# Performance work log

Hardware: AMD Instinct MI355X
Metric: run time of the kernel (lower is better)

Reference implementation:

```python
import jax, jax.numpy as jnp
import numpy as np

IN, E, BSZ, A, J, NC, BATCH = 784, 512, 8, 2, 7, 128, 512
T = BSZ ** A  # 64 blocks


def setup_inputs() -> dict:
    key = jax.random.key(0)
    ks = jax.random.split(key, 10)
    s = lambda k, sh: (jax.random.normal(k, sh, jnp.float32) * 0.02)
    return {
        "x": jax.random.normal(ks[0], (BATCH, IN), jnp.float32),
        "emb_W": s(ks[1], (IN, E)), "emb_b": jnp.zeros((E,), jnp.float32),
        # stacked per-block state_transform: Linear(E,E)-ReLU-Linear(E,E)-ReLU
        "st_W1": s(ks[2], (T, E, E)), "st_b1": jnp.zeros((T, E), jnp.float32),
        "st_W2": s(ks[3], (T, E, E)), "st_b2": jnp.zeros((T, E), jnp.float32),
        # stacked per-block address_transform: Linear(E,E)-ReLU-Linear(E,A*BSZ)
        "ad_W1": s(ks[4], (T, E, E)), "ad_b1": jnp.zeros((T, E), jnp.float32),
        "ad_W2": s(ks[5], (T, E, A * BSZ)), "ad_b2": jnp.zeros((T, A * BSZ), jnp.float32),
        # output head: Linear(E,E)-ReLU-Linear(E,NC)
        "out_W1": s(ks[6], (E, E)), "out_b1": jnp.zeros((E,), jnp.float32),
        "out_W2": s(ks[7], (E, NC)), "out_b2": jnp.zeros((NC,), jnp.float32),
    }


def reference(x, emb_W, emb_b, st_W1, st_b1, st_W2, st_b2,
              ad_W1, ad_b1, ad_W2, ad_b2, out_W1, out_b1, out_W2, out_b2):
    strides = BSZ ** jnp.arange(A - 1, -1, -1)  # row-major flat index

    def flat_idx(addr):  # [B, A] -> [B]
        return jnp.sum(addr * strides, axis=1)

    def next_address(state, idx):
        # block's address_transform; argmax(softmax(logits)) == argmax(logits)
        h = jax.nn.relu(jnp.einsum("be,beh->bh", state, ad_W1[idx]) + ad_b1[idx])
        logits = jnp.einsum("bh,bho->bo", h, ad_W2[idx]) + ad_b2[idx]
        return jnp.argmax(logits.reshape(-1, A, BSZ), axis=2)  # [B, A]

    def through_block(state, idx):
        h = jax.nn.relu(jnp.einsum("be,beh->bh", state, st_W1[idx]) + st_b1[idx])
        t = jax.nn.relu(jnp.einsum("bh,bho->bo", h, st_W2[idx]) + st_b2[idx])
        norm = jnp.linalg.norm(state, axis=1, keepdims=True)
        return t / (norm + 1e-6)

    state = x.reshape(x.shape[0], -1) @ emb_W + emb_b  # [B, E]
    initial_state = state
    B = state.shape[0]
    # initial address from brain_blocks[0]
    addr = next_address(initial_state, jnp.zeros((B,), jnp.int32))

    for i in range(J):  # small fixed jump count
        idx = flat_idx(addr)
        t = through_block(state, idx)           # normalized transformed state
        addr = next_address(t, idx)             # address from transformed state
        state = t + (i / max(1, J - 1)) * initial_state  # residual ramp

    final = through_block(state, flat_idx(addr)) + initial_state
    h = jax.nn.relu(final @ out_W1 + out_b1)
    return h @ out_W2 + out_b2  # [B, NC]
```

## Files before the change

kernel.cpp:

```cpp
#include <hip/hip_runtime.h>

namespace {

constexpr int B     = 512;
constexpr int IN_F  = 784;
constexpr int E     = 512;
constexpr int ABSZ  = 16;
constexpr int J     = 7;
constexpr int NC    = 128;
constexpr int NT    = 256;

__device__ inline void matvec512(const float* __restrict__ W,
                                 const float* __restrict__ bias,
                                 const float* __restrict__ vin,
                                 float* __restrict__ vout,
                                 int tid, bool do_relu)
{
    const int o = 2 * tid;
    float a0 = 0.f, a1 = 0.f;
    const float* wp = W + o;
    #pragma unroll 8
    for (int e = 0; e < E; ++e) {
        const float v = vin[e];
        const float2 w = *reinterpret_cast<const float2*>(wp + (size_t)e * E);
        a0 = fmaf(v, w.x, a0);
        a1 = fmaf(v, w.y, a1);
    }
    a0 += bias[o];
    a1 += bias[o + 1];
    if (do_relu) { a0 = fmaxf(a0, 0.f); a1 = fmaxf(a1, 0.f); }
    vout[o]     = a0;
    vout[o + 1] = a1;
}

__device__ inline int next_address(const float* __restrict__ ad_W1,
                                   const float* __restrict__ ad_b1,
                                   const float* __restrict__ ad_W2,
                                   const float* __restrict__ ad_b2,
                                   int idx,
                                   const float* __restrict__ vin,
                                   float* __restrict__ s_h,
                                   float* __restrict__ s_part,
                                   float* __restrict__ s_logits,
                                   int* __restrict__ s_idx_p,
                                   int tid)
{
    matvec512(ad_W1 + (size_t)idx * E * E, ad_b1 + (size_t)idx * E, vin, s_h, tid, true);
    __syncthreads();

    {
        const int o  = tid & (ABSZ - 1);
        const int e0 = tid >> 4;
        const float* w2 = ad_W2 + (size_t)idx * E * ABSZ;
        float acc = 0.f;
        #pragma unroll 4
        for (int e = e0; e < E; e += 16) {
            acc = fmaf(s_h[e], w2[(size_t)e * ABSZ + o], acc);
        }
        s_part[tid] = acc;
    }
    __syncthreads();
    if (tid < ABSZ) {
        float sum = ad_b2[(size_t)idx * ABSZ + tid];
        #pragma unroll
        for (int k = 0; k < 16; ++k) sum += s_part[tid + 16 * k];
        s_logits[tid] = sum;
    }
    __syncthreads();
    if (tid == 0) {
        int a0 = 0, a1 = 0;
        float m0 = s_logits[0], m1 = s_logits[8];
        #pragma unroll
        for (int k = 1; k < 8; ++k) {
            if (s_logits[k]     > m0) { m0 = s_logits[k];     a0 = k; }
            if (s_logits[8 + k] > m1) { m1 = s_logits[8 + k]; a1 = k; }
        }
        *s_idx_p = a0 * 8 + a1;
    }
    __syncthreads();
    return *s_idx_p;
}

__device__ inline void through_block(const float* __restrict__ st_W1,
                                     const float* __restrict__ st_b1,
                                     const float* __restrict__ st_W2,
                                     const float* __restrict__ st_b2,
                                     int idx,
                                     const float* __restrict__ s_state,
                                     float* __restrict__ s_h,
                                     float* __restrict__ s_t,
                                     float* __restrict__ s_part,
                                     float* __restrict__ s_scale,
                                     int tid)
{
    matvec512(st_W1 + (size_t)idx * E * E, st_b1 + (size_t)idx * E, s_state, s_h, tid, true);

    {
        const int o = 2 * tid;
        float v0 = s_state[o], v1 = s_state[o + 1];
        float ss = v0 * v0 + v1 * v1;
        #pragma unroll
        for (int off = 32; off > 0; off >>= 1) ss += __shfl_down(ss, off, 64);
        if ((tid & 63) == 0) s_part[tid >> 6] = ss;
    }
    __syncthreads();
    if (tid == 0) {
        float tot = s_part[0] + s_part[1] + s_part[2] + s_part[3];
        *s_scale = 1.0f / (sqrtf(tot) + 1e-6f);
    }
    matvec512(st_W2 + (size_t)idx * E * E, st_b2 + (size_t)idx * E, s_h, s_t, tid, true);
    __syncthreads();
    {
        const float sc = *s_scale;
        const int o = 2 * tid;
        s_t[o]     *= sc;
        s_t[o + 1] *= sc;
    }
    __syncthreads();
}

__global__ __launch_bounds__(NT) void brain_kernel(
    const float* __restrict__ x,
    const float* __restrict__ emb_W,  const float* __restrict__ emb_b,
    const float* __restrict__ st_W1,  const float* __restrict__ st_b1,
    const float* __restrict__ st_W2,  const float* __restrict__ st_b2,
    const float* __restrict__ ad_W1,  const float* __restrict__ ad_b1,
    const float* __restrict__ ad_W2,  const float* __restrict__ ad_b2,
    const float* __restrict__ out_W1, const float* __restrict__ out_b1,
    const float* __restrict__ out_W2, const float* __restrict__ out_b2,
    float* __restrict__ out)
{
    const int b   = blockIdx.x;
    const int tid = threadIdx.x;

    __shared__ float s_x[IN_F];
    __shared__ float s_state[E];
    __shared__ float s_init[E];
    __shared__ float s_h[E];
    __shared__ float s_t[E];
    __shared__ float s_part[NT];
    __shared__ float s_logits[ABSZ];
    __shared__ float s_scale;
    __shared__ int   s_idx;

    for (int i = tid; i < IN_F; i += NT) s_x[i] = x[(size_t)b * IN_F + i];
    __syncthreads();

    {
        const int o = 2 * tid;
        float a0 = 0.f, a1 = 0.f;
        const float* wp = emb_W + o;
        #pragma unroll 4
        for (int i = 0; i < IN_F; ++i) {
            const float v = s_x[i];
            const float2 w = *reinterpret_cast<const float2*>(wp + (size_t)i * E);
            a0 = fmaf(v, w.x, a0);
            a1 = fmaf(v, w.y, a1);
        }
        a0 += emb_b[o];
        a1 += emb_b[o + 1];
        s_state[o]     = a0;  s_state[o + 1] = a1;
        s_init[o]      = a0;  s_init[o + 1]  = a1;
    }
    __syncthreads();

    int idx = next_address(ad_W1, ad_b1, ad_W2, ad_b2, 0, s_init,
                           s_h, s_part, s_logits, &s_idx, tid);

    for (int i = 0; i < J; ++i) {
        through_block(st_W1, st_b1, st_W2, st_b2, idx,
                      s_state, s_h, s_t, s_part, &s_scale, tid);
        const int nidx = next_address(ad_W1, ad_b1, ad_W2, ad_b2, idx, s_t,
                                      s_h, s_part, s_logits, &s_idx, tid);
        {
            const float ramp = (float)i * (1.0f / 6.0f);
            const int o = 2 * tid;
            s_state[o]     = s_t[o]     + ramp * s_init[o];
            s_state[o + 1] = s_t[o + 1] + ramp * s_init[o + 1];
        }
        __syncthreads();
        idx = nidx;
    }

    through_block(st_W1, st_b1, st_W2, st_b2, idx,
                  s_state, s_h, s_t, s_part, &s_scale, tid);
    {
        const int o = 2 * tid;
        s_state[o]     = s_t[o]     + s_init[o];
        s_state[o + 1] = s_t[o + 1] + s_init[o + 1];
    }
    __syncthreads();

    matvec512(out_W1, out_b1, s_state, s_h, tid, true);
    __syncthreads();

    {
        const int oo = tid & (NC - 1);
        const int e0 = tid >> 7;
        float acc = 0.f;
        #pragma unroll 4
        for (int e = e0; e < E; e += 2) {
            acc = fmaf(s_h[e], out_W2[(size_t)e * NC + oo], acc);
        }
        s_part[tid] = acc;
    }
    __syncthreads();
    if (tid < NC) {
        out[(size_t)b * NC + tid] = out_b2[tid] + s_part[tid] + s_part[tid + NC];
    }
}

}

extern "C" void kernel_launch(void* const* d_in, const int* in_sizes, int n_in,
                              void* d_out, int out_size, void* d_ws, size_t ws_size,
                              hipStream_t stream)
{
    const float* x      = (const float*)d_in[0];
    const float* emb_W  = (const float*)d_in[1];
    const float* emb_b  = (const float*)d_in[2];
    const float* st_W1  = (const float*)d_in[3];
    const float* st_b1  = (const float*)d_in[4];
    const float* st_W2  = (const float*)d_in[5];
    const float* st_b2  = (const float*)d_in[6];
    const float* ad_W1  = (const float*)d_in[7];
    const float* ad_b1  = (const float*)d_in[8];
    const float* ad_W2  = (const float*)d_in[9];
    const float* ad_b2  = (const float*)d_in[10];
    const float* out_W1 = (const float*)d_in[11];
    const float* out_b1 = (const float*)d_in[12];
    const float* out_W2 = (const float*)d_in[13];
    const float* out_b2 = (const float*)d_in[14];
    float* out = (float*)d_out;

    hipLaunchKernelGGL(brain_kernel, dim3(B), dim3(NT), 0, stream,
                       x, emb_W, emb_b, st_W1, st_b1, st_W2, st_b2,
                       ad_W1, ad_b1, ad_W2, ad_b2,
                       out_W1, out_b1, out_W2, out_b2, out);
}
```

Measured before the change: 1.755 ms.

## Bucket rows by block index and run persistent cooperative kernel with 8-row tiled matvecs

Replaces the one-workgroup-per-sample kernel with a persistent cooperative kernel that runs stage by stage, separated by grid syncs. Before each jump it buckets samples by their chosen block index, so each workgroup processes up to 8 rows that share the same weight matrix and reuses every loaded weight column across those rows. This cuts the redundant weight streaming the per-sample approach incurred. In exchange it adds many grid-wide barriers, global workspace traffic for intermediate activations, and partially filled tiles when buckets are small.

```diff
diff --git a/kernel.cpp b/kernel.cpp
--- a/kernel.cpp
+++ b/kernel.cpp
@@ -1,212 +1,361 @@
 #include <hip/hip_runtime.h>
+#include <hip/hip_cooperative_groups.h>
+
+namespace cg = cooperative_groups;
 
 namespace {
 
-constexpr int B     = 512;
-constexpr int IN_F  = 784;
-constexpr int E     = 512;
-constexpr int ABSZ  = 16;
-constexpr int J     = 7;
-constexpr int NC    = 128;
-constexpr int NT    = 256;
-
-__device__ inline void matvec512(const float* __restrict__ W,
-                                 const float* __restrict__ bias,
-                                 const float* __restrict__ vin,
-                                 float* __restrict__ vout,
-                                 int tid, bool do_relu)
-{
-    const int o = 2 * tid;
-    float a0 = 0.f, a1 = 0.f;
-    const float* wp = W + o;
-    #pragma unroll 8
-    for (int e = 0; e < E; ++e) {
-        const float v = vin[e];
-        const float2 w = *reinterpret_cast<const float2*>(wp + (size_t)e * E);
-        a0 = fmaf(v, w.x, a0);
-        a1 = fmaf(v, w.y, a1);
-    }
-    a0 += bias[o];
-    a1 += bias[o + 1];
-    if (do_relu) { a0 = fmaxf(a0, 0.f); a1 = fmaxf(a1, 0.f); }
-    vout[o]     = a0;
-    vout[o + 1] = a1;
-}
-
-__device__ inline int next_address(const float* __restrict__ ad_W1,
-                                   const float* __restrict__ ad_b1,
-                                   const float* __restrict__ ad_W2,
-                                   const float* __restrict__ ad_b2,
-                                   int idx,
-                                   const float* __restrict__ vin,
-                                   float* __restrict__ s_h,
-                                   float* __restrict__ s_part,
-                                   float* __restrict__ s_logits,
-                                   int* __restrict__ s_idx_p,
-                                   int tid)
-{
-    matvec512(ad_W1 + (size_t)idx * E * E, ad_b1 + (size_t)idx * E, vin, s_h, tid, true);
+constexpr int Bn   = 512;
+constexpr int INF  = 784;
+constexpr int E    = 512;
+constexpr int Tn   = 64;
+constexpr int ABSZ = 16;
+constexpr int Jn   = 7;
+constexpr int NC   = 128;
+constexpr int NT   = 256;
+constexpr int DESCMAX = 128;
+
+struct Params {
+    const float *x, *emb_W, *emb_b;
+    const float *st_W1, *st_b1, *st_W2, *st_b2;
+    const float *ad_W1, *ad_b1, *ad_W2, *ad_b2;
+    const float *out_W1, *out_b1, *out_W2, *out_b2;
+    float *out;
+    float *state, *initv, *hbuf, *tbuf, *norms;
+    int *idx, *g_rlist;
+    int4 *g_desc;
+};
+
+__device__ inline void stage_rows(const float* __restrict__ in, int instride,
+                                  int kb, int klen, const int* rid,
+                                  float (*s_in)[E], int tid)
+{
+    #pragma unroll
+    for (int g = 0; g < 8; ++g) {
+        const float* src = in + (size_t)rid[g] * instride + kb;
+        float* dst = s_in[g];
+        for (int e4 = tid; e4 < (klen >> 2); e4 += NT)
+            reinterpret_cast<float4*>(dst)[e4] =
+                reinterpret_cast<const float4*>(src)[e4];
+    }
+}
+
+__device__ inline void accum8(const float* __restrict__ Wp,
+                              const float (*s_in)[E], int klen, float acc[8])
+{
+    #pragma unroll 2
+    for (int e = 0; e < klen; e += 4) {
+        const float w0 = Wp[(size_t)(e + 0) * E];
+        const float w1 = Wp[(size_t)(e + 1) * E];
+        const float w2 = Wp[(size_t)(e + 2) * E];
+        const float w3 = Wp[(size_t)(e + 3) * E];
+        #pragma unroll
+        for (int g = 0; g < 8; ++g) {
+            const float4 f = *reinterpret_cast<const float4*>(&s_in[g][e]);
+            acc[g] = fmaf(f.x, w0, acc[g]);
+            acc[g] = fmaf(f.y, w1, acc[g]);
+            acc[g] = fmaf(f.z, w2, acc[g]);
+            acc[g] = fmaf(f.w, w3, acc[g]);
+        }
+    }
+}
+
+__device__ inline int build_buckets(const int* __restrict__ gidx,
+                                    int* cnt, int* off, int* rk, int* tb,
+                                    int* rlist, int4* sdesc,
+                                    int tid, bool pub, const Params& P)
+{
+    if (tid < Tn) { cnt[tid] = 0; rk[tid] = 0; }
     __syncthreads();
-
-    {
-        const int o  = tid & (ABSZ - 1);
-        const int e0 = tid >> 4;
-        const float* w2 = ad_W2 + (size_t)idx * E * ABSZ;
-        float acc = 0.f;
-        #pragma unroll 4
-        for (int e = e0; e < E; e += 16) {
-            acc = fmaf(s_h[e], w2[(size_t)e * ABSZ + o], acc);
-        }
-        s_part[tid] = acc;
-    }
-    __syncthreads();
-    if (tid < ABSZ) {
-        float sum = ad_b2[(size_t)idx * ABSZ + tid];
-        #pragma unroll
-        for (int k = 0; k < 16; ++k) sum += s_part[tid + 16 * k];
-        s_logits[tid] = sum;
-    }
+    int rv[2];
+    #pragma unroll
+    for (int k = 0; k < 2; ++k) rv[k] = gidx[tid + k * NT];
+    #pragma unroll
+    for (int k = 0; k < 2; ++k) atomicAdd(&cnt[rv[k]], 1);
     __syncthreads();
     if (tid == 0) {
-        int a0 = 0, a1 = 0;
-        float m0 = s_logits[0], m1 = s_logits[8];
-        #pragma unroll
-        for (int k = 1; k < 8; ++k) {
-            if (s_logits[k]     > m0) { m0 = s_logits[k];     a0 = k; }
-            if (s_logits[8 + k] > m1) { m1 = s_logits[8 + k]; a1 = k; }
-        }
-        *s_idx_p = a0 * 8 + a1;
+        int s = 0, t = 0;
+        for (int b = 0; b < Tn; ++b) {
+            off[b] = s; tb[b] = t;
+            s += cnt[b]; t += (cnt[b] + 7) >> 3;
+        }
+        tb[Tn] = t;
     }
     __syncthreads();
-    return *s_idx_p;
-}
-
-__device__ inline void through_block(const float* __restrict__ st_W1,
-                                     const float* __restrict__ st_b1,
-                                     const float* __restrict__ st_W2,
-                                     const float* __restrict__ st_b2,
-                                     int idx,
-                                     const float* __restrict__ s_state,
-                                     float* __restrict__ s_h,
-                                     float* __restrict__ s_t,
-                                     float* __restrict__ s_part,
-                                     float* __restrict__ s_scale,
-                                     int tid)
-{
-    matvec512(st_W1 + (size_t)idx * E * E, st_b1 + (size_t)idx * E, s_state, s_h, tid, true);
+    #pragma unroll
+    for (int k = 0; k < 2; ++k) {
+        const int r = tid + k * NT, b = rv[k];
+        rlist[off[b] + atomicAdd(&rk[b], 1)] = r;
+    }
+    __syncthreads();
+    const int nt = tb[Tn];
+    for (int t = tid; t < DESCMAX; t += NT) {
+        int4 d = make_int4(0, 0, 0, 0);
+        if (t < nt) {
+            int b = 0;
+            while (tb[b + 1] <= t) ++b;
+            const int j = t - tb[b];
+            d = make_int4(b, off[b] + j * 8, min(8, cnt[b] - j * 8), 0);
+        }
+        sdesc[t] = d;
+    }
+    __syncthreads();
+    if (pub) {
+        for (int r = tid; r < Bn; r += NT) P.g_rlist[r] = rlist[r];
+        for (int t = tid; t < DESCMAX; t += NT) P.g_desc[t] = sdesc[t];
+    }
+    return nt;
+}
+
+enum { EPI_EMBED, EPI_H, EPI_T, EPI_FINAL };
+
+template <int EPI>
+__device__ void stage_mv(const Params& P, const float* __restrict__ in,
+                         int instride, int K,
+                         const float* __restrict__ W, const float* __restrict__ bias,
+                         bool gathered, int ntiles,
+                         const int* __restrict__ rl, const int4* __restrict__ dsc,
+                         float* __restrict__ outp,
+                         float (*s_in)[E], int tid, int bid, int gridn)
+{
+    const int items = ntiles * 2;
+    for (int s = bid; s < items; s += gridn) {
+        const int tile = s >> 1, chunk = s & 1;
+        int blk = 0, start = tile * 8, n = 8;
+        if (gathered) {
+            const int4 d = dsc[tile];
+            blk = d.x; start = d.y; n = d.z;
+            if (n == 0) continue;
+        }
+        int rid[8];
+        #pragma unroll
+        for (int g = 0; g < 8; ++g)
+            rid[g] = gathered ? rl[start + min(g, n - 1)] : (start + g);
+
+        float acc[8] = {0, 0, 0, 0, 0, 0, 0, 0};
+        for (int kb = 0; kb < K; kb += E) {
+            const int klen = min(E, K - kb);
+            __syncthreads();
+            stage_rows(in, instride, kb, klen, rid, s_in, tid);
+            __syncthreads();
+            const float* Wp = W + (size_t)blk * K * E + (size_t)kb * E
+                              + (chunk * NT + tid);
+            accum8(Wp, s_in, klen, acc);
+        }
+        const int c = chunk * NT + tid;
+        const float bv = bias[(gathered ? blk * E : 0) + c];
+        #pragma unroll
+        for (int g = 0; g < 8; ++g) {
+            if (g < n) {
+                float v = acc[g] + bv;
+                const size_t o = (size_t)rid[g] * E + c;
+                if (EPI == EPI_EMBED) {
+                    P.state[o] = v; P.initv[o] = v;
+                } else if (EPI == EPI_H) {
+                    outp[o] = fmaxf(v, 0.f);
+                } else if (EPI == EPI_T) {
+                    outp[o] = fmaxf(v, 0.f) / (P.norms[rid[g]] + 1e-6f);
+                } else {
+                    P.state[o] = fmaxf(v, 0.f) / (P.norms[rid[g]] + 1e-6f)
+                                 + P.initv[o];
+                }
+            }
+        }
+    }
+}
+
+template <bool UPDATE>
+__device__ void stage_addr(const Params& P, const float* __restrict__ in,
+                           float ramp, bool gathered, int ntiles,
+                           const int* __restrict__ rl, const int4* __restrict__ dsc,
+                           float (*s_in)[E], float* slog,
+                           int tid, int bid, int gridn)
+{
+    for (int s = bid; s < ntiles; s += gridn) {
+        int blk = 0, start = s * 8, n = 8;
+        if (gathered) {
+            const int4 d = dsc[s];
+            blk = d.x; start = d.y; n = d.z;
+            if (n == 0) continue;
+        }
+        int rid[8];
+        #pragma unroll
+        for (int g = 0; g < 8; ++g)
+            rid[g] = gathered ? rl[start + min(g, n - 1)] : (start + g);
+
+        __syncthreads();
+        stage_rows(in, E, 0, E, rid, s_in, tid);
+        __syncthreads();
+
+        const float* W1 = P.ad_W1 + (size_t)blk * E * E;
+        float a0[8] = {0, 0, 0, 0, 0, 0, 0, 0};
+        float a1[8] = {0, 0, 0, 0, 0, 0, 0, 0};
+        #pragma unroll 2
+        for (int e = 0; e < E; e += 4) {
+            float w0[4], w1v[4];
+            #pragma unroll
+            for (int q = 0; q < 4; ++q) {
+                w0[q]  = W1[(size_t)(e + q) * E + tid];
+                w1v[q] = W1[(size_t)(e + q) * E + tid + NT];
+            }
+            #pragma unroll
+            for (int g = 0; g < 8; ++g) {
+                const float4 f = *reinterpret_cast<const float4*>(&s_in[g][e]);
+                a0[g] = fmaf(f.x, w0[0], a0[g]);
+                a0[g] = fmaf(f.y, w0[1], a0[g]);
+                a0[g] = fmaf(f.z, w0[2], a0[g]);
+                a0[g] = fmaf(f.w, w0[3], a0[g]);
+                a1[g] = fmaf(f.x, w1v[0], a1[g]);
+                a1[g] = fmaf(f.y, w1v[1], a1[g]);
+                a1[g] = fmaf(f.z, w1v[2], a1[g]);
+                a1[g] = fmaf(f.w, w1v[3], a1[g]);
+            }
+        }
+
+        {
+            const int g = tid >> 5, l = tid & 31;
+            if (g < n) {
+                const int r = rid[g];
+                float ss = 0.f;
+                const int e0 = l * 16;
+                #pragma unroll
+                for (int e = e0; e < e0 + 16; e += 4) {
+                    float4 tv = *reinterpret_cast<const float4*>(&s_in[g][e]);
+                    if (UPDATE) {
+                        const float4 iv = *reinterpret_cast<const float4*>(
+                            &P.initv[(size_t)r * E + e]);
+                        tv.x = fmaf(ramp, iv.x, tv.x);
+                        tv.y = fmaf(ramp, iv.y, tv.y);
+                        tv.z = fmaf(ramp, iv.z, tv.z);
+                        tv.w = fmaf(ramp, iv.w, tv.w);
+                        *reinterpret_cast<float4*>(&P.state[(size_t)r * E + e]) = tv;
+                    }
+                    ss += tv.x * tv.x + tv.y * tv.y + tv.z * tv.z + tv.w * tv.w;
+                }
+                #pragma unroll
+                for (int m = 16; m > 0; m >>= 1) ss += __shfl_xor(ss, m, 64);
+                if (l == 0) P.norms[r] = sqrtf(ss);
+            }
+        }
+        __syncthreads();
+
+        const float bb0 = P.ad_b1[blk * E + tid];
+        const float bb1 = P.ad_b1[blk * E + tid + NT];
+        #pragma unroll
+        for (int g = 0; g < 8; ++g) {
+            s_in[g][tid]      = fmaxf(a0[g] + bb0, 0.f);
+            s_in[g][tid + NT] = fmaxf(a1[g] + bb1, 0.f);
+        }
+        __syncthreads();
+
+        {
+            const int d = tid >> 1, half = tid & 1;
+            const int row = d >> 4, o = d & 15;
+            const float* W2 = P.ad_W2 + (size_t)blk * E * ABSZ;
+            float lacc = 0.f;
+            const int e0 = half * 256;
+            #pragma unroll 4
+            for (int e = e0; e < e0 + 256; ++e)
+                lacc = fmaf(s_in[row][e], W2[(size_t)e * ABSZ + o], lacc);
+            lacc += __shfl_xor(lacc, 1, 64);
+            if (half == 0) slog[d] = lacc + P.ad_b2[blk * ABSZ + o];
+        }
+        __syncthreads();
+        if (tid < n) {
+            const float* L = slog + tid * ABSZ;
+            int A0 = 0, A1 = 0;
+            float m0 = L[0], m1 = L[8];
+            #pragma unroll
+            for (int k = 1; k < 8; ++k) {
+                if (L[k]     > m0) { m0 = L[k];     A0 = k; }
+                if (L[8 + k] > m1) { m1 = L[8 + k]; A1 = k; }
+            }
+            P.idx[rid[tid]] = A0 * 8 + A1;
+        }
+        __syncthreads();
+    }
+}
+
+__global__ __launch_bounds__(NT, 2) void brain_fused(Params P)
+{
+    cg::grid_group grid = cg::this_grid();
+    const int tid = threadIdx.x, bid = blockIdx.x, gridn = gridDim.x;
+
+    __shared__ float s_in[8][E];
+    __shared__ int   rlist[Bn];
+    __shared__ int4  sdesc[DESCMAX];
+    __shared__ int   cnt[Tn], off[Tn], rk[Tn], tb[Tn + 1];
+    __shared__ float slog[8 * ABSZ];
+
+    stage_mv<EPI_EMBED>(P, P.x, INF, INF, P.emb_W, P.emb_b,
+                        false, Bn / 8, nullptr, nullptr, nullptr,
+                        s_in, tid, bid, gridn);
+    grid.sync();
+
+    stage_addr<false>(P, P.initv, 0.f, false, Bn / 8, nullptr, nullptr,
+                      s_in, slog, tid, bid, gridn);
+    grid.sync();
+
+    for (int i = 0; i < Jn; ++i) {
+        const int nt = build_buckets(P.idx, cnt, off, rk, tb, rlist, sdesc,
+                                     tid, bid == 0, P);
+        stage_mv<EPI_H>(P, P.state, E, E, P.st_W1, P.st_b1,
+                        true, nt, rlist, sdesc, P.hbuf,
+                        s_in, tid, bid, gridn);
+        grid.sync();
+        stage_mv<EPI_T>(P, P.hbuf, E, E, P.st_W2, P.st_b2,
+                        true, nt, P.g_rlist, P.g_desc, P.tbuf,
+                        s_in, tid, bid, gridn);
+        grid.sync();
+        stage_addr<true>(P, P.tbuf, (float)i * (1.0f / 6.0f),
+                         true, nt, P.g_rlist, P.g_desc,
+                         s_in, slog, tid, bid, gridn);
+        grid.sync();
+    }
 
     {
-        const int o = 2 * tid;
-        float v0 = s_state[o], v1 = s_state[o + 1];
-        float ss = v0 * v0 + v1 * v1;
-        #pragma unroll
-        for (int off = 32; off > 0; off >>= 1) ss += __shfl_down(ss, off, 64);
-        if ((tid & 63) == 0) s_part[tid >> 6] = ss;
-    }
-    __syncthreads();
-    if (tid == 0) {
-        float tot = s_part[0] + s_part[1] + s_part[2] + s_part[3];
-        *s_scale = 1.0f / (sqrtf(tot) + 1e-6f);
-    }
-    matvec512(st_W2 + (size_t)idx * E * E, st_b2 + (size_t)idx * E, s_h, s_t, tid, true);
-    __syncthreads();
-    {
-        const float sc = *s_scale;
-        const int o = 2 * tid;
-        s_t[o]     *= sc;
-        s_t[o + 1] *= sc;
-    }
-    __syncthreads();
-}
-
-__global__ __launch_bounds__(NT) void brain_kernel(
-    const float* __restrict__ x,
-    const float* __restrict__ emb_W,  const float* __restrict__ emb_b,
-    const float* __restrict__ st_W1,  const float* __restrict__ st_b1,
-    const float* __restrict__ st_W2,  const float* __restrict__ st_b2,
-    const float* __restrict__ ad_W1,  const float* __restrict__ ad_b1,
-    const float* __restrict__ ad_W2,  const float* __restrict__ ad_b2,
-    const float* __restrict__ out_W1, const float* __restrict__ out_b1,
-    const float* __restrict__ out_W2, const float* __restrict__ out_b2,
-    float* __restrict__ out)
-{
-    const int b   = blockIdx.x;
-    const int tid = threadIdx.x;
-
-    __shared__ float s_x[IN_F];
-    __shared__ float s_state[E];
-    __shared__ float s_init[E];
-    __shared__ float s_h[E];
-    __shared__ float s_t[E];
-    __shared__ float s_part[NT];
-    __shared__ float s_logits[ABSZ];
-    __shared__ float s_scale;
-    __shared__ int   s_idx;
-
-    for (int i = tid; i < IN_F; i += NT) s_x[i] = x[(size_t)b * IN_F + i];
-    __syncthreads();
-
-    {
-        const int o = 2 * tid;
-        float a0 = 0.f, a1 = 0.f;
-        const float* wp = emb_W + o;
+        const int nt = build_buckets(P.idx, cnt, off, rk, tb, rlist, sdesc,
+                                     tid, bid == 0, P);
+        stage_mv<EPI_H>(P, P.state, E, E, P.st_W1, P.st_b1,
+                        true, nt, rlist, sdesc, P.hbuf,
+                        s_in, tid, bid, gridn);
+        grid.sync();
+        stage_mv<EPI_FINAL>(P, P.hbuf, E, E, P.st_W2, P.st_b2,
+                            true, nt, P.g_rlist, P.g_desc, nullptr,
+                            s_in, tid, bid, gridn);
+        grid.sync();
+    }
+
+    stage_mv<EPI_H>(P, P.state, E, E, P.out_W1, P.out_b1,
+                    false, Bn / 8, nullptr, nullptr, P.hbuf,
+                    s_in, tid, bid, gridn);
+    grid.sync();
+
+    for (int s = bid; s < Bn / 8; s += gridn) {
+        const int base = s * 8;
+        int rid[8];
+        #pragma unroll
+        for (int g = 0; g < 8; ++g) rid[g] = base + g;
+        __syncthreads();
+        stage_rows(P.hbuf, E, 0, E, rid, s_in, tid);
+        __syncthreads();
+        const int col = tid & (NC - 1), rg = tid >> 7;
+        float acc[4] = {0, 0, 0, 0};
         #pragma unroll 4
-        for (int i = 0; i < IN_F; ++i) {
-            const float v = s_x[i];
-            const float2 w = *reinterpret_cast<const float2*>(wp + (size_t)i * E);
-            a0 = fmaf(v, w.x, a0);
-            a1 = fmaf(v, w.y, a1);
-        }
-        a0 += emb_b[o];
-        a1 += emb_b[o + 1];
-        s_state[o]     = a0;  s_state[o + 1] = a1;
-        s_init[o]      = a0;  s_init[o + 1]  = a1;
-    }
-    __syncthreads();
-
-    int idx = next_address(ad_W1, ad_b1, ad_W2, ad_b2, 0, s_init,
-                           s_h, s_part, s_logits, &s_idx, tid);
-
-    for (int i = 0; i < J; ++i) {
-        through_block(st_W1, st_b1, st_W2, st_b2, idx,
-                      s_state, s_h, s_t, s_part, &s_scale, tid);
-        const int nidx = next_address(ad_W1, ad_b1, ad_W2, ad_b2, idx, s_t,
-                                      s_h, s_part, s_logits, &s_idx, tid);
-        {
-            const float ramp = (float)i * (1.0f / 6.0f);
-            const int o = 2 * tid;
-            s_state[o]     = s_t[o]     + ramp * s_init[o];
-            s_state[o + 1] = s_t[o + 1] + ramp * s_init[o + 1];
-        }
-        __syncthreads();
-        idx = nidx;
-    }
-
-    through_block(st_W1, st_b1, st_W2, st_b2, idx,
-                  s_state, s_h, s_t, s_part, &s_scale, tid);
-    {
-        const int o = 2 * tid;
-        s_state[o]     = s_t[o]     + s_init[o];
-        s_state[o + 1] = s_t[o + 1] + s_init[o + 1];
-    }
-    __syncthreads();
-
-    matvec512(out_W1, out_b1, s_state, s_h, tid, true);
-    __syncthreads();
-
-    {
-        const int oo = tid & (NC - 1);
-        const int e0 = tid >> 7;
-        float acc = 0.f;
-        #pragma unroll 4
-        for (int e = e0; e < E; e += 2) {
-            acc = fmaf(s_h[e], out_W2[(size_t)e * NC + oo], acc);
-        }
-        s_part[tid] = acc;
-    }
-    __syncthreads();
-    if (tid < NC) {
-        out[(size_t)b * NC + tid] = out_b2[tid] + s_part[tid] + s_part[tid + NC];
+        for (int e = 0; e < E; e += 2) {
+            const float w0 = P.out_W2[(size_t)e * NC + col];
+            const float w1 = P.out_W2[(size_t)(e + 1) * NC + col];
+            #pragma unroll
+            for (int j = 0; j < 4; ++j) {
+                const int g = rg * 4 + j;
+                acc[j] = fmaf(s_in[g][e], w0, acc[j]);
+                acc[j] = fmaf(s_in[g][e + 1], w1, acc[j]);
+            }
+        }
+        const float bv = P.out_b2[col];
+        #pragma unroll
+        for (int j = 0; j < 4; ++j)
+            P.out[(size_t)(base + rg * 4 + j) * NC + col] = acc[j] + bv;
     }
 }
 
@@ -216,25 +365,41 @@
                               void* d_out, int out_size, void* d_ws, size_t ws_size,
                               hipStream_t stream)
 {
-    const float* x      = (const float*)d_in[0];
-    const float* emb_W  = (const float*)d_in[1];
-    const float* emb_b  = (const float*)d_in[2];
-    const float* st_W1  = (const float*)d_in[3];
-    const float* st_b1  = (const float*)d_in[4];
-    const float* st_W2  = (const float*)d_in[5];
-    const float* st_b2  = (const float*)d_in[6];
-    const float* ad_W1  = (const float*)d_in[7];
-    const float* ad_b1  = (const float*)d_in[8];
-    const float* ad_W2  = (const float*)d_in[9];
-    const float* ad_b2  = (const float*)d_in[10];
-    const float* out_W1 = (const float*)d_in[11];
-    const float* out_b1 = (const float*)d_in[12];
-    const float* out_W2 = (const float*)d_in[13];
-    const float* out_b2 = (const float*)d_in[14];
-    float* out = (float*)d_out;
-
-    hipLaunchKernelGGL(brain_kernel, dim3(B), dim3(NT), 0, stream,
-                       x, emb_W, emb_b, st_W1, st_b1, st_W2, st_b2,
-                       ad_W1, ad_b1, ad_W2, ad_b2,
-                       out_W1, out_b1, out_W2, out_b2, out);
-}
+    Params p;
+    p.x      = (const float*)d_in[0];
+    p.emb_W  = (const float*)d_in[1];
+    p.emb_b  = (const float*)d_in[2];
+    p.st_W1  = (const float*)d_in[3];
+    p.st_b1  = (const float*)d_in[4];
+    p.st_W2  = (const float*)d_in[5];
+    p.st_b2  = (const float*)d_in[6];
+    p.ad_W1  = (const float*)d_in[7];
+    p.ad_b1  = (const float*)d_in[8];
+    p.ad_W2  = (const float*)d_in[9];
+    p.ad_b2  = (const float*)d_in[10];
+    p.out_W1 = (const float*)d_in[11];
+    p.out_b1 = (const float*)d_in[12];
+    p.out_W2 = (const float*)d_in[13];
+    p.out_b2 = (const float*)d_in[14];
+    p.out    = (float*)d_out;
+
+    float* ws = (float*)d_ws;
+    p.state = ws;
+    p.initv = ws + 1 * 262144;
+    p.hbuf  = ws + 2 * 262144;
+    p.tbuf  = ws + 3 * 262144;
+    p.norms = ws + 4 * 262144;
+    p.idx     = (int*)(p.norms + Bn);
+    p.g_rlist = p.idx + Bn;
+    p.g_desc  = (int4*)(p.g_rlist + Bn);
+
+    int occ = 0;
+    hipOccupancyMaxActiveBlocksPerMultiprocessor(&occ, brain_fused, NT, 0);
+    if (occ < 1) occ = 1;
+    int grid = occ * 256;
+    if (grid > 512) grid = 512;
+
+    void* args[] = { &p };
+    hipLaunchCooperativeKernel((const void*)brain_fused, dim3(grid), dim3(NT),
+                               args, 0, stream);
+}
```

Result: slower. 2.783 ms (+58.6%).
